# Kernel optimization log

Hardware: AMD Instinct MI355X
Metric: run time of the kernel (lower is better)

## Reference

```python
import jax, jax.numpy as jnp
import numpy as np

B, T, A, D = 256, 2048, 22, 2
MAX_GAP = 512  # max NaN-gap length injected per row


def setup_inputs() -> dict:
    key = jax.random.key(0)
    k1, k2, k3 = jax.random.split(key, 3)
    x = jax.random.normal(k1, (B, T, A, D), dtype=jnp.float32)
    # one contiguous NaN gap per row: frames (s, e) exclusive are NaN
    s = jax.random.randint(k2, (B,), 1, T // 2)        # last valid frame before gap
    gap = jax.random.randint(k3, (B,), 1, MAX_GAP)     # gap length
    e = s + gap + 1                                    # first valid frame after gap
    t = jnp.arange(T)
    gap_mask = (t[None, :] > s[:, None]) & (t[None, :] < e[:, None])  # [B, T]
    x = jnp.where(gap_mask[:, :, None, None], jnp.nan, x)
    return {"x": x}


def reference(x):
    # x: [B, T, A, D] with one contiguous NaN gap along T per row.
    Bn, Tn = x.shape[0], x.shape[1]
    nan_mask = jnp.isnan(x).reshape(Bn, Tn, -1).any(axis=2)       # [B, T]
    start = jnp.argmax(nan_mask, axis=1) - 1                       # last valid before gap
    end = Tn - jnp.argmax(nan_mask[:, ::-1], axis=1)               # first valid after gap

    b = jnp.arange(Bn)
    x_s = x[b, start]                                              # [B, A, D]
    x_e = x[b, end]                                                # [B, A, D]

    t = jnp.arange(Tn)[None, :]                                    # [1, T]
    # weight at frame t is (t - s) / (e - s), matching linspace(0,1,gap+2)[1:-1]
    w = (t - start[:, None]).astype(x.dtype) / (end - start)[:, None].astype(x.dtype)
    w = w[:, :, None, None]                                        # [B, T, 1, 1]
    interp = x_s[:, None] * (1.0 - w) + x_e[:, None] * w           # [B, T, A, D]

    in_gap = (t > start[:, None]) & (t < end[:, None])             # [B, T]
    return jnp.where(in_gap[:, :, None, None], interp, x)
```

## Files before the change

kernel.cpp:

```cpp
#include <hip/hip_runtime.h>

#define BB 256
#define TT 2048
#define AD4 11
#define F4_PER_B (TT * AD4)
#define NTHREADS 1024
#define HALF 11
#define NWAVES (NTHREADS / 64)

typedef float v4 __attribute__((ext_vector_type(4)));

__global__ __launch_bounds__(NTHREADS) void interp_fused(
    const v4* __restrict__ x4, v4* __restrict__ out4) {
  const int tid = threadIdx.x;
  const int b = blockIdx.x;
  const size_t base = (size_t)b * F4_PER_B;

  int tmin = TT;
  int tmax = -1;

#pragma unroll
  for (int h = 0; h < 2; ++h) {
    const int hbase = h * (HALF * NTHREADS);
    v4 v[HALF];
#pragma unroll
    for (int k = 0; k < HALF; ++k) {
      v[k] = x4[base + hbase + k * NTHREADS + tid];
    }
#pragma unroll
    for (int k = 0; k < HALF; ++k) {
      const int off = hbase + k * NTHREADS + tid;
      const v4 w = v[k];
      const bool n = (w.x != w.x) || (w.y != w.y) || (w.z != w.z) || (w.w != w.w);
      if (!n) {
        out4[base + off] = w;
      } else {
        const int t = off / AD4;
        tmin = min(tmin, t);
        tmax = max(tmax, t);
      }
    }
  }

#pragma unroll
  for (int d = 32; d > 0; d >>= 1) {
    tmin = min(tmin, __shfl_xor(tmin, d));
    tmax = max(tmax, __shfl_xor(tmax, d));
  }

  __shared__ int smin[NWAVES], smax[NWAVES];
  __shared__ int s_sh, e_sh;
  const int wid = tid >> 6;
  if ((tid & 63) == 0) {
    smin[wid] = tmin;
    smax[wid] = tmax;
  }
  __syncthreads();
  if (tid == 0) {
    int a = TT, z = -1;
#pragma unroll
    for (int i = 0; i < NWAVES; ++i) {
      a = min(a, smin[i]);
      z = max(z, smax[i]);
    }
    if (z < 0) {
      s_sh = 0;
      e_sh = 1;
    } else {
      s_sh = a - 1;
      e_sh = z + 1;
    }
  }
  __syncthreads();
  const int s = s_sh;
  const int e = e_sh;

  __shared__ v4 sxs[AD4], sxe[AD4];
  if (tid < AD4) sxs[tid] = x4[base + (size_t)s * AD4 + tid];
  if (tid >= 64 && tid < 64 + AD4) sxe[tid - 64] = x4[base + (size_t)e * AD4 + (tid - 64)];
  __syncthreads();

  const float inv = 1.0f / (float)(e - s);
  const int total = (e - s - 1) * AD4;
  for (int i = tid; i < total; i += NTHREADS) {
    const int dt = i / AD4;
    const int c = i - dt * AD4;
    const int t = s + 1 + dt;
    const float w = (float)(dt + 1) * inv;
    const float om = 1.0f - w;
    const v4 a = sxs[c];
    const v4 z = sxe[c];
    v4 r;
    r.x = a.x * om + z.x * w;
    r.y = a.y * om + z.y * w;
    r.z = a.z * om + z.z * w;
    r.w = a.w * om + z.w * w;
    out4[base + (size_t)t * AD4 + c] = r;
  }
}

extern "C" void kernel_launch(void* const* d_in, const int* in_sizes, int n_in,
                              void* d_out, int out_size, void* d_ws, size_t ws_size,
                              hipStream_t stream) {
  const v4* x4 = (const v4*)d_in[0];
  v4* out4 = (v4*)d_out;
  interp_fused<<<BB, NTHREADS, 0, stream>>>(x4, out4);
}
```

Before: 166.5 us.

## Split copy and gap-fill into separate block roles with strided NaN scan

Replaces the one-block-per-row fused kernel with a grid of many 256-thread blocks. Most blocks only copy non-NaN float4s using nontemporal stores, while one block per row finds the gap. That block reads only the first float of each frame to locate the gap, then writes the interpolated values. This spreads the bandwidth-bound copy over far more blocks than the 256 large blocks before, and it relies on any NaN frame having its first element NaN.

```diff
diff --git a/kernel.cpp b/kernel.cpp
--- a/kernel.cpp
+++ b/kernel.cpp
@@ -2,43 +2,59 @@
 
 #define BB 256
 #define TT 2048
+#define AD 44
 #define AD4 11
 #define F4_PER_B (TT * AD4)
-#define NTHREADS 1024
-#define HALF 11
-#define NWAVES (NTHREADS / 64)
+#define ELEMS 8
+#define BLK_F4 (256 * ELEMS)
+#define BLOCKS_PER_B 11
+#define NCOPY (BB * BLOCKS_PER_B)
+#define NBLK (BB + NCOPY)
 
 typedef float v4 __attribute__((ext_vector_type(4)));
 
-__global__ __launch_bounds__(NTHREADS) void interp_fused(
-    const v4* __restrict__ x4, v4* __restrict__ out4) {
+__global__ __launch_bounds__(256) void interp_split(const v4* __restrict__ x4,
+                                                    v4* __restrict__ out4) {
   const int tid = threadIdx.x;
-  const int b = blockIdx.x;
-  const size_t base = (size_t)b * F4_PER_B;
 
-  int tmin = TT;
-  int tmax = -1;
+  if (blockIdx.x >= BB) {
+    const int cid = blockIdx.x - BB;
+    const int b = cid / BLOCKS_PER_B;
+    const int blk_in_b = cid - b * BLOCKS_PER_B;
+    const size_t base = (size_t)b * F4_PER_B + blk_in_b * BLK_F4;
 
+    v4 v[ELEMS];
 #pragma unroll
-  for (int h = 0; h < 2; ++h) {
-    const int hbase = h * (HALF * NTHREADS);
-    v4 v[HALF];
-#pragma unroll
-    for (int k = 0; k < HALF; ++k) {
-      v[k] = x4[base + hbase + k * NTHREADS + tid];
+    for (int k = 0; k < ELEMS; ++k) {
+      v[k] = x4[base + k * 256 + tid];
     }
 #pragma unroll
-    for (int k = 0; k < HALF; ++k) {
-      const int off = hbase + k * NTHREADS + tid;
+    for (int k = 0; k < ELEMS; ++k) {
       const v4 w = v[k];
       const bool n = (w.x != w.x) || (w.y != w.y) || (w.z != w.z) || (w.w != w.w);
       if (!n) {
-        out4[base + off] = w;
-      } else {
-        const int t = off / AD4;
-        tmin = min(tmin, t);
-        tmax = max(tmax, t);
+        __builtin_nontemporal_store(w, &out4[base + k * 256 + tid]);
       }
+    }
+    return;
+  }
+
+  const int b = blockIdx.x;
+  const float* xf = (const float*)x4;
+  const size_t fbase = (size_t)b * (TT * AD);
+
+  float c[8];
+#pragma unroll
+  for (int k = 0; k < 8; ++k) {
+    c[k] = xf[fbase + (size_t)(k * 256 + tid) * AD];
+  }
+  int tmin = TT, tmax = -1;
+#pragma unroll
+  for (int k = 0; k < 8; ++k) {
+    if (c[k] != c[k]) {
+      const int t = k * 256 + tid;
+      tmin = min(tmin, t);
+      tmax = max(tmax, t);
     }
   }
 
@@ -47,8 +63,7 @@
     tmin = min(tmin, __shfl_xor(tmin, d));
     tmax = max(tmax, __shfl_xor(tmax, d));
   }
-
-  __shared__ int smin[NWAVES], smax[NWAVES];
+  __shared__ int smin[4], smax[4];
   __shared__ int s_sh, e_sh;
   const int wid = tid >> 6;
   if ((tid & 63) == 0) {
@@ -59,7 +74,7 @@
   if (tid == 0) {
     int a = TT, z = -1;
 #pragma unroll
-    for (int i = 0; i < NWAVES; ++i) {
+    for (int i = 0; i < 4; ++i) {
       a = min(a, smin[i]);
       z = max(z, smax[i]);
     }
@@ -76,26 +91,27 @@
   const int e = e_sh;
 
   __shared__ v4 sxs[AD4], sxe[AD4];
+  const size_t base = (size_t)b * F4_PER_B;
   if (tid < AD4) sxs[tid] = x4[base + (size_t)s * AD4 + tid];
   if (tid >= 64 && tid < 64 + AD4) sxe[tid - 64] = x4[base + (size_t)e * AD4 + (tid - 64)];
   __syncthreads();
 
   const float inv = 1.0f / (float)(e - s);
   const int total = (e - s - 1) * AD4;
-  for (int i = tid; i < total; i += NTHREADS) {
+  for (int i = tid; i < total; i += 256) {
     const int dt = i / AD4;
-    const int c = i - dt * AD4;
+    const int cch = i - dt * AD4;
     const int t = s + 1 + dt;
     const float w = (float)(dt + 1) * inv;
     const float om = 1.0f - w;
-    const v4 a = sxs[c];
-    const v4 z = sxe[c];
+    const v4 a = sxs[cch];
+    const v4 z = sxe[cch];
     v4 r;
     r.x = a.x * om + z.x * w;
     r.y = a.y * om + z.y * w;
     r.z = a.z * om + z.z * w;
     r.w = a.w * om + z.w * w;
-    out4[base + (size_t)t * AD4 + c] = r;
+    out4[base + (size_t)t * AD4 + cch] = r;
   }
 }
 
@@ -104,5 +120,5 @@
                               hipStream_t stream) {
   const v4* x4 = (const v4*)d_in[0];
   v4* out4 = (v4*)d_out;
-  interp_fused<<<BB, NTHREADS, 0, stream>>>(x4, out4);
+  interp_split<<<NBLK, 256, 0, stream>>>(x4, out4);
 }
```

Measured after the change: 171.7 us. +3.1%, slower.
